# Kernel optimization log

Hardware: AMD Instinct MI355X
Metric: run time of the kernel (lower is better)

The kernel has to match this reference:

```python
import jax, jax.numpy as jnp
import numpy as np

N = 5000        # nodes
F = 7699        # node feature dim (fixed by code)
E = 40000       # edges
ED = 3          # edge_dim (fixed by code)
H1, C1 = 4, 1024
H2, C2 = 1, 1024
NUM_OUT = 128
NEG_SLOPE = 0.2


def _glorot(key, shape):
    fan_in = shape[0]
    return jax.random.normal(key, shape, jnp.float32) / np.float32(np.sqrt(fan_in))


def setup_inputs() -> dict:
    key = jax.random.key(0)
    ks = jax.random.split(key, 16)
    x = jax.random.normal(ks[0], (N, F), jnp.float32)
    src = jax.random.randint(ks[1], (E,), 0, N)
    dst = jax.random.randint(ks[2], (E,), 0, N)
    src = jnp.where(src == dst, (src + 1) % N, src)  # no pre-existing self loops
    edge_index = jnp.stack([src, dst]).astype(jnp.int32)
    edge_attr = jax.random.normal(ks[3], (E, ED), jnp.float32)
    inp = {
        "x": x, "edge_index": edge_index, "edge_attr": edge_attr,
        # GATv2Conv #1: 7699 -> 1024, heads=4, edge_dim=3
        "W1l": _glorot(ks[4], (F, H1 * C1)), "b1l": jnp.zeros((H1 * C1,), jnp.float32),
        "W1r": _glorot(ks[5], (F, H1 * C1)), "b1r": jnp.zeros((H1 * C1,), jnp.float32),
        "W1e": _glorot(ks[6], (ED, H1 * C1)),
        "att1": _glorot(ks[7], (H1, C1)),
        "bias1": jnp.zeros((H1 * C1,), jnp.float32),
        # GATv2Conv #2: 4096 -> 1024, heads=1, edge_dim=3
        "W2l": _glorot(ks[8], (H1 * C1, H2 * C2)), "b2l": jnp.zeros((H2 * C2,), jnp.float32),
        "W2r": _glorot(ks[9], (H1 * C1, H2 * C2)), "b2r": jnp.zeros((H2 * C2,), jnp.float32),
        "W2e": _glorot(ks[10], (ED, H2 * C2)),
        "att2": _glorot(ks[11], (H2, C2)),
        "bias2": jnp.zeros((H2 * C2,), jnp.float32),
        # final Linear(1024, num_outputs)
        "Wlin": _glorot(ks[12], (C2, NUM_OUT)), "blin": jnp.zeros((NUM_OUT,), jnp.float32),
    }
    return inp


def gatv2_layer(x, src, dst, edge_attr, Wl, bl, Wr, br, We, att, bias, heads, out_ch):
    """PyG GATv2Conv with add_self_loops=True, fill_value='mean', concat=True."""
    n = x.shape[0]
    # self-loop edge_attr = mean of incoming edge attrs per node (fill_value='mean')
    deg = jax.ops.segment_sum(jnp.ones((src.shape[0],), jnp.float32), dst, num_segments=n)
    loop_attr = jax.ops.segment_sum(edge_attr, dst, num_segments=n) / jnp.maximum(deg, 1.0)[:, None]
    idx = jnp.arange(n, dtype=src.dtype)
    srcf = jnp.concatenate([src, idx])
    dstf = jnp.concatenate([dst, idx])
    ea = jnp.concatenate([edge_attr, loop_attr], axis=0)
    xl = (x @ Wl + bl).reshape(n, heads, out_ch)   # lin_l (source)
    xr = (x @ Wr + br).reshape(n, heads, out_ch)   # lin_r (target)
    ee = (ea @ We).reshape(-1, heads, out_ch)       # lin_edge (no bias)
    e = jax.nn.leaky_relu(xl[srcf] + xr[dstf] + ee, NEG_SLOPE)  # [E', H, C]
    logit = jnp.einsum('ehc,hc->eh', e, att)                     # [E', H]
    # segment softmax over destination nodes (every node has a self loop)
    m = jax.lax.stop_gradient(jax.ops.segment_max(logit, dstf, num_segments=n))
    a = jnp.exp(logit - m[dstf])
    denom = jax.ops.segment_sum(a, dstf, num_segments=n)
    alpha = a / (denom[dstf] + 1e-16)
    out = jax.ops.segment_sum(alpha[:, :, None] * xl[srcf], dstf, num_segments=n)  # [N,H,C]
    return out.reshape(n, heads * out_ch) + bias


def reference(x, edge_index, edge_attr,
              W1l, b1l, W1r, b1r, W1e, att1, bias1,
              W2l, b2l, W2r, b2r, W2e, att2, bias2,
              Wlin, blin):
    src, dst = edge_index[0], edge_index[1]
    h = gatv2_layer(x, src, dst, edge_attr, W1l, b1l, W1r, b1r, W1e, att1, bias1, H1, C1)
    h = gatv2_layer(h, src, dst, edge_attr, W2l, b2l, W2r, b2r, W2e, att2, bias2, H2, C2)
    return h @ Wlin + blin
```

## Files before the change

kernel.cpp:

```cpp
#include <hip/hip_runtime.h>
#include <cstdint>
#include <cstddef>

#define N_NODES 5000
#define F_IN    7699
#define KP1     7712
#define KT1     241
#define MP      5120
#define E_EDGES 40000
#define EFULL   45000
#define HC1     4096
#define N1      8192
#define HC2     1024
#define N2      2048
#define NOUT    128
#define GM256   (MP / 256)
#define GM128   (MP / 128)

typedef __bf16 bf16x8 __attribute__((ext_vector_type(8)));
typedef float  f32x4  __attribute__((ext_vector_type(4)));
typedef float  f32x16 __attribute__((ext_vector_type(16)));
typedef unsigned short u16x8 __attribute__((ext_vector_type(8)));
typedef _Float16 f16;
typedef _Float16 f16x8 __attribute__((ext_vector_type(8)));

using as1_uchar = unsigned char __attribute__((address_space(1)));
using as3_uchar = unsigned char __attribute__((address_space(3)));

__device__ __forceinline__ unsigned short f2bf(float f) {
  union { float f; unsigned int u; } v; v.f = f;
  return (unsigned short)((v.u + 0x7fffu + ((v.u >> 16) & 1u)) >> 16);
}
__device__ __forceinline__ float bf2f(unsigned short h) {
  union { unsigned int u; float f; } v; v.u = ((unsigned int)h) << 16;
  return v.f;
}

__device__ __forceinline__ void gload16(const void* g, void* l) {
  __builtin_amdgcn_global_load_lds(
      reinterpret_cast<const as1_uchar*>(reinterpret_cast<uintptr_t>(g)),
      reinterpret_cast<as3_uchar*>(reinterpret_cast<uintptr_t>(l)),
      16, 0, 0);
}



__global__ void k_split_x(const float* __restrict__ x, unsigned short* __restrict__ hi,
                          unsigned short* __restrict__ lo) {
  const int C8 = KP1 / 8;
  int ci = blockIdx.x * 256 + threadIdx.x;
  if (ci >= MP * C8) return;
  int r = ci / C8, c8 = ci % C8;
  int c = c8 * 8;
  u16x8 hb, lb;
  #pragma unroll
  for (int j = 0; j < 8; ++j) {
    float v = 0.f;
    if (r < N_NODES && (c + j) < F_IN) v = x[(size_t)r * F_IN + c + j];
    unsigned short h = f2bf(v);
    hb[j] = h; lb[j] = f2bf(v - bf2f(h));
  }
  size_t off = ((size_t)((r >> 7) * KT1 + (c >> 5)) * 4 + ((c >> 3) & 3)) * 1024 + (r & 127) * 8;
  *(u16x8*)&hi[off] = hb;
  *(u16x8*)&lo[off] = lb;
}


__global__ void k_split_w(const float* __restrict__ W,
                          unsigned short* __restrict__ hi, unsigned short* __restrict__ lo,
                          int K, int Nsrc, int c0, int KT, int rowOffset) {
  __shared__ float tile[32][33];
  const int tid = threadIdx.x;
  const int kt = blockIdx.x;
  const int n0 = blockIdx.y * 32;
  #pragma unroll
  for (int i = tid >> 5; i < 32; i += 8) {
    int k = kt * 32 + i;
    tile[i][tid & 31] = (k < K) ? W[(size_t)k * Nsrc + c0 + n0 + (tid & 31)] : 0.f;
  }
  __syncthreads();
  if (tid < 128) {
    const int nn = tid >> 2, kc = (tid & 3) << 3;
    const int n = rowOffset + n0 + nn;
    u16x8 hb, lb;
    #pragma unroll
    for (int j = 0; j < 8; ++j) {
      float v = tile[kc + j][nn];
      unsigned short h = f2bf(v);
      hb[j] = h; lb[j] = f2bf(v - bf2f(h));
    }
    size_t off = ((size_t)((n >> 7) * KT + kt) * 4 + (kc >> 3)) * 1024 + (n & 127) * 8;
    *(u16x8*)&hi[off] = hb;
    *(u16x8*)&lo[off] = lb;
  }
}


template <int OF16>
__global__ __launch_bounds__(512, 2) void k_gemm_big(
    const unsigned short* __restrict__ Ahi, const unsigned short* __restrict__ Alo,
    const unsigned short* __restrict__ Bhi, const unsigned short* __restrict__ Blo,
    void* __restrict__ Cp, const float* __restrict__ bias0, const float* __restrict__ bias1,
    int halfN, int M, int Nc, int ldC, int KT32, int nbn)
{
  __shared__ __align__(16) unsigned short S[4 * 12288];

  const int tid = threadIdx.x;
  const int lane = tid & 63;
  const int w = tid >> 6;
  const int wm = w >> 1, wn = w & 1;

  const int nwg = gridDim.x;
  const int qq = nwg >> 3, rr = nwg & 7;
  const int xcd = blockIdx.x & 7, idx = blockIdx.x >> 3;
  const int wg = (xcd < rr ? xcd * (qq + 1) : rr * (qq + 1) + (xcd - rr) * qq) + idx;
  const int bm = wg / nbn, bn = wg % nbn;

  f32x16 acc[2][2] = {};

  const unsigned short* gsrc[3];
  int dd[3];
  #pragma unroll
  for (int s = 0; s < 3; ++s) {
    const int q = w * 3 + s;
    const unsigned short* base; int dOff; size_t rowoff; int p, hf;
    if (q < 8)       { int r_ = q;      base = Ahi; int t = r_ >> 2; p = (r_ >> 1) & 1; hf = r_ & 1;
                       dOff = t * 2048 + p * 1024 + hf * 512; rowoff = (size_t)(bm * 2 + t) * KT32 * 4096; }
    else if (q < 16) { int r_ = q - 8;  base = Alo; int t = r_ >> 2; p = (r_ >> 1) & 1; hf = r_ & 1;
                       dOff = 4096 + t * 2048 + p * 1024 + hf * 512; rowoff = (size_t)(bm * 2 + t) * KT32 * 4096; }
    else if (q < 20) { int r_ = q - 16; base = Bhi; p = (r_ >> 1) & 1; hf = r_ & 1;
                       dOff = 8192 + p * 1024 + hf * 512; rowoff = (size_t)bn * KT32 * 4096; }
    else             { int r_ = q - 20; base = Blo; p = (r_ >> 1) & 1; hf = r_ & 1;
                       dOff = 10240 + p * 1024 + hf * 512; rowoff = (size_t)bn * KT32 * 4096; }
    gsrc[s] = base + rowoff + p * 1024 + hf * 512 + lane * 8;
    dd[s] = dOff;
  }

  auto stage = [&](int kt16, int bufo) {
    const size_t o = (size_t)kt16 * 2048;
    #pragma unroll
    for (int s = 0; s < 3; ++s) gload16(gsrc[s] + o, &S[bufo + dd[s]]);
  };

  const int r5 = lane & 31, h5 = lane >> 5;
  const int tA = wm >> 1;
  const int rrA = (wm & 1) * 64;
  int ra[2], cb[2];
  #pragma unroll
  for (int i = 0; i < 2; ++i) ra[i] = tA * 2048 + h5 * 1024 + (rrA + i * 32 + r5) * 8;
  #pragma unroll
  for (int j = 0; j < 2; ++j) cb[j] = 8192 + h5 * 1024 + (wn * 64 + j * 32 + r5) * 8;

  struct Frags { bf16x8 ah[2], al[2], bh[2], bl[2]; };
  auto rdfr = [&](Frags& f, int bufo) {
    #pragma unroll
    for (int i = 0; i < 2; ++i) {
      f.ah[i] = *(const bf16x8*)&S[bufo + ra[i]];
      f.al[i] = *(const bf16x8*)&S[bufo + 4096 + ra[i]];
    }
    #pragma unroll
    for (int j = 0; j < 2; ++j) {
      f.bh[j] = *(const bf16x8*)&S[bufo + cb[j]];
      f.bl[j] = *(const bf16x8*)&S[bufo + 2048 + cb[j]];
    }
  };
  auto domfma = [&](Frags& f) {
    __builtin_amdgcn_s_setprio(1);
    #pragma unroll
    for (int j = 0; j < 2; ++j)
      #pragma unroll
      for (int i = 0; i < 2; ++i) {
        acc[i][j] = __builtin_amdgcn_mfma_f32_32x32x16_bf16(f.ah[i], f.bh[j], acc[i][j], 0, 0, 0);
        acc[i][j] = __builtin_amdgcn_mfma_f32_32x32x16_bf16(f.al[i], f.bh[j], acc[i][j], 0, 0, 0);
        acc[i][j] = __builtin_amdgcn_mfma_f32_32x32x16_bf16(f.ah[i], f.bl[j], acc[i][j], 0, 0, 0);
      }
    __builtin_amdgcn_s_setprio(0);
  };

  const int KT16 = KT32 * 2;

  stage(0, 0);
  stage(1, 12288);
  stage(2, 24576);
  asm volatile("s_waitcnt vmcnt(3)" ::: "memory");
  __builtin_amdgcn_s_barrier();
  Frags fA, fB;
  rdfr(fA, 0);

  int o0 = 0, o1 = 12288, o2 = 24576, o3 = 36864;
  for (int kt = 0; kt < KT16; kt += 2) {
    stage((kt + 3 < KT16) ? kt + 3 : KT16 - 1, o3);
    rdfr(fB, o1);
    domfma(fA);
    asm volatile("s_waitcnt vmcnt(3)" ::: "memory");
    __builtin_amdgcn_s_barrier();
    stage((kt + 4 < KT16) ? kt + 4 : KT16 - 1, o0);
    rdfr(fA, o2);
    domfma(fB);
    asm volatile("s_waitcnt vmcnt(3)" ::: "memory");
    __builtin_amdgcn_s_barrier();
    int t0 = o0, t1 = o1;
    o0 = o2; o1 = o3; o2 = t0; o3 = t1;
  }

  #pragma unroll
  for (int i = 0; i < 2; ++i) {
    #pragma unroll
    for (int j = 0; j < 2; ++j) {
      const int gc = bn * 128 + wn * 64 + j * 32 + r5;
      if (gc < Nc) {
        const float bv = (gc < halfN) ? bias0[gc] : bias1[gc - halfN];
        #pragma unroll
        for (int reg = 0; reg < 16; ++reg) {
          const int gr = bm * 256 + wm * 64 + i * 32 + (reg & 3) + 8 * (reg >> 2) + 4 * h5;
          if (gr < M) {
            float v = acc[i][j][reg] + bv;
            if (OF16) ((f16*)Cp)[(size_t)gr * ldC + gc] = (f16)v;
            else      ((float*)Cp)[(size_t)gr * ldC + gc] = v;
          }
        }
      }
    }
  }
}


template <int OF16>
__global__ __launch_bounds__(256, 2) void k_gemm_bb(
    const unsigned short* __restrict__ Ahi, const unsigned short* __restrict__ Alo,
    const unsigned short* __restrict__ Bhi, const unsigned short* __restrict__ Blo,
    void* __restrict__ Cp, const float* __restrict__ bias0, const float* __restrict__ bias1,
    int halfN, int M, int Nc, int ldC, int KT32, int nbn)
{
  __shared__ __align__(16) unsigned short S[4 * 8192];

  const int tid = threadIdx.x;
  const int lane = tid & 63;
  const int w = tid >> 6;
  const int wm = w >> 1, wn = w & 1;

  const int nwg = gridDim.x;
  const int qq = nwg >> 3, rr = nwg & 7;
  const int xcd = blockIdx.x & 7, idx = blockIdx.x >> 3;
  const int wg = (xcd < rr ? xcd * (qq + 1) : rr * (qq + 1) + (xcd - rr) * qq) + idx;
  const int bm = wg / nbn, bn = wg % nbn;

  f32x16 acc[2][2] = {};

  const unsigned short* gbase = (w == 0) ? Ahi : (w == 1) ? Alo : (w == 2) ? Bhi : Blo;
  const int brow = (w < 2) ? bm : bn;
  const unsigned short* gsrc[4];
  int dd[4];
  #pragma unroll
  for (int s = 0; s < 4; ++s) {
    const int p = s >> 1, hf = s & 1;
    gsrc[s] = gbase + (size_t)brow * KT32 * 4096 + p * 1024 + hf * 512 + lane * 8;
    dd[s] = w * 2048 + p * 1024 + hf * 512;
  }

  auto stage = [&](int kt16, int bufo) {
    const size_t o = (size_t)kt16 * 2048;
    #pragma unroll
    for (int s = 0; s < 4; ++s) gload16(gsrc[s] + o, &S[bufo + dd[s]]);
  };

  const int r5 = lane & 31, h5 = lane >> 5;
  int ra[2], cb[2];
  #pragma unroll
  for (int i = 0; i < 2; ++i) ra[i] = h5 * 1024 + (wm * 64 + i * 32 + r5) * 8;
  #pragma unroll
  for (int j = 0; j < 2; ++j) cb[j] = 4096 + h5 * 1024 + (wn * 64 + j * 32 + r5) * 8;

  struct Frags { bf16x8 ah[2], al[2], bh[2], bl[2]; };
  auto rdfr = [&](Frags& f, int bufo) {
    #pragma unroll
    for (int i = 0; i < 2; ++i) {
      f.ah[i] = *(const bf16x8*)&S[bufo + ra[i]];
      f.al[i] = *(const bf16x8*)&S[bufo + 2048 + ra[i]];
    }
    #pragma unroll
    for (int j = 0; j < 2; ++j) {
      f.bh[j] = *(const bf16x8*)&S[bufo + cb[j]];
      f.bl[j] = *(const bf16x8*)&S[bufo + 2048 + cb[j]];
    }
  };
  auto domfma = [&](Frags& f) {
    __builtin_amdgcn_s_setprio(1);
    #pragma unroll
    for (int j = 0; j < 2; ++j)
      #pragma unroll
      for (int i = 0; i < 2; ++i) {
        acc[i][j] = __builtin_amdgcn_mfma_f32_32x32x16_bf16(f.ah[i], f.bh[j], acc[i][j], 0, 0, 0);
        acc[i][j] = __builtin_amdgcn_mfma_f32_32x32x16_bf16(f.al[i], f.bh[j], acc[i][j], 0, 0, 0);
        acc[i][j] = __builtin_amdgcn_mfma_f32_32x32x16_bf16(f.ah[i], f.bl[j], acc[i][j], 0, 0, 0);
      }
    __builtin_amdgcn_s_setprio(0);
  };

  const int KT16 = KT32 * 2;

  stage(0, 0);
  stage(1, 8192);
  stage(2, 16384);
  asm volatile("s_waitcnt vmcnt(4)" ::: "memory");
  __builtin_amdgcn_s_barrier();
  Frags fA, fB;
  rdfr(fA, 0);

  int o0 = 0, o1 = 8192, o2 = 16384, o3 = 24576;
  for (int kt = 0; kt < KT16; kt += 2) {
    stage((kt + 3 < KT16) ? kt + 3 : KT16 - 1, o3);
    rdfr(fB, o1);
    domfma(fA);
    asm volatile("s_waitcnt vmcnt(4)" ::: "memory");
    __builtin_amdgcn_s_barrier();
    stage((kt + 4 < KT16) ? kt + 4 : KT16 - 1, o0);
    rdfr(fA, o2);
    domfma(fB);
    asm volatile("s_waitcnt vmcnt(4)" ::: "memory");
    __builtin_amdgcn_s_barrier();
    int t0 = o0, t1 = o1;
    o0 = o2; o1 = o3; o2 = t0; o3 = t1;
  }

  #pragma unroll
  for (int i = 0; i < 2; ++i) {
    #pragma unroll
    for (int j = 0; j < 2; ++j) {
      const int gc = bn * 128 + wn * 64 + j * 32 + r5;
      if (gc < Nc) {
        const float bv = (gc < halfN) ? bias0[gc] : bias1[gc - halfN];
        #pragma unroll
        for (int reg = 0; reg < 16; ++reg) {
          const int gr = bm * 128 + wm * 64 + i * 32 + (reg & 3) + 8 * (reg >> 2) + 4 * h5;
          if (gr < M) {
            float v = acc[i][j][reg] + bv;
            if (OF16) ((f16*)Cp)[(size_t)gr * ldC + gc] = (f16)v;
            else      ((float*)Cp)[(size_t)gr * ldC + gc] = v;
          }
        }
      }
    }
  }
}


__global__ void k_deg(const int* __restrict__ dst, const float* __restrict__ ea,
                      float* __restrict__ deg, float* __restrict__ lattr, int E) {
  int e = blockIdx.x * 256 + threadIdx.x;
  if (e >= E) return;
  int d = dst[e];
  atomicAdd(&deg[d], 1.f);
  atomicAdd(&lattr[d * 3 + 0], ea[e * 3 + 0]);
  atomicAdd(&lattr[d * 3 + 1], ea[e * 3 + 1]);
  atomicAdd(&lattr[d * 3 + 2], ea[e * 3 + 2]);
}

__global__ void k_lattr_fin(float* __restrict__ lattr, const float* __restrict__ deg, int n) {
  int i = blockIdx.x * 256 + threadIdx.x;
  if (i >= n) return;
  float dv = fmaxf(deg[i], 1.f);
  lattr[i * 3 + 0] /= dv; lattr[i * 3 + 1] /= dv; lattr[i * 3 + 2] /= dv;
}

__global__ void k_eafull(const float* __restrict__ ea, const float* __restrict__ lattr,
                         float* __restrict__ eaf, int E, int n) {
  int e = blockIdx.x * 256 + threadIdx.x;
  if (e >= E + n) return;
  const float* s = (e < E) ? &ea[(size_t)e * 3] : &lattr[(size_t)(e - E) * 3];
  eaf[e * 3 + 0] = s[0]; eaf[e * 3 + 1] = s[1]; eaf[e * 3 + 2] = s[2];
}

__global__ void k_count(const int* __restrict__ dst, int* __restrict__ cnt, int E, int n) {
  int e = blockIdx.x * 256 + threadIdx.x;
  if (e >= E + n) return;
  int d = (e < E) ? dst[e] : (e - E);
  atomicAdd(&cnt[d], 1);
}

__global__ void k_scan(const int* __restrict__ cnt, int* __restrict__ rowptr, int n) {
  int lane = threadIdx.x;
  int run = 0;
  for (int base = 0; base < n; base += 64) {
    int i = base + lane;
    int v = (i < n) ? cnt[i] : 0;
    #pragma unroll
    for (int off = 1; off < 64; off <<= 1) {
      int t = __shfl_up(v, off, 64);
      if (lane >= off) v += t;
    }
    if (i < n) rowptr[i + 1] = run + v;
    run += __shfl(v, 63, 64);
  }
  if (lane == 0) rowptr[0] = 0;
}

__global__ void k_fill(const int* __restrict__ dst, const int* __restrict__ rowptr,
                       int* __restrict__ fillc, int* __restrict__ elist, int E, int n) {
  int e = blockIdx.x * 256 + threadIdx.x;
  if (e >= E + n) return;
  int d = (e < E) ? dst[e] : (e - E);
  int pos = rowptr[d] + atomicAdd(&fillc[d], 1);
  elist[pos] = e;
}


template <int H, int ITERS>
__global__ __launch_bounds__(256) void k_logit_stats(
    const f16* __restrict__ xl, const f16* __restrict__ xr, int strideX,
    const float* __restrict__ eaf, const float* __restrict__ We, const float* __restrict__ att,
    const int* __restrict__ rowptr, const int* __restrict__ elist, const int* __restrict__ src,
    int E, float* __restrict__ logit, float* __restrict__ mb, float* __restrict__ db)
{
  const int n = blockIdx.x;
  const int tid = threadIdx.x;
  constexpr int HC = ITERS * 256;
  float xrv[ITERS], w0[ITERS], w1[ITERS], w2[ITERS], av[ITERS];
  const f16* rr = xr + (size_t)n * strideX;
  #pragma unroll
  for (int i = 0; i < ITERS; ++i) {
    const int hc = tid + (i << 8);
    xrv[i] = (float)rr[hc];
    w0[i] = We[hc]; w1[i] = We[HC + hc]; w2[i] = We[2 * HC + hc];
    av[i] = att[hc];
  }
  const int start = rowptr[n], end = rowptr[n + 1];
  __shared__ float red[H][4];
  const int lane = tid & 63, wv = tid >> 6;
  float mh = -1e30f, sh = 0.f;

  for (int p = start; p < end; ++p) {
    const int e = elist[p];
    const int s = (e < E) ? src[e] : (e - E);
    const float ea0 = eaf[e * 3 + 0], ea1 = eaf[e * 3 + 1], ea2 = eaf[e * 3 + 2];
    const f16* rl = xl + (size_t)s * strideX;
    float acc[H];
    #pragma unroll
    for (int h = 0; h < H; ++h) acc[h] = 0.f;
    #pragma unroll
    for (int i = 0; i < ITERS; ++i) {
      const int hc = tid + (i << 8);
      float v = (float)rl[hc] + xrv[i] + ea0 * w0[i] + ea1 * w1[i] + ea2 * w2[i];
      v = (v > 0.f) ? v : 0.2f * v;
      acc[i >> 2] += v * av[i];
    }
    #pragma unroll
    for (int h = 0; h < H; ++h) {
      float v = acc[h];
      #pragma unroll
      for (int off = 32; off > 0; off >>= 1) v += __shfl_down(v, off, 64);
      if (lane == 0) red[h][wv] = v;
    }
    __syncthreads();
    if (tid < H) {
      const float l = red[tid][0] + red[tid][1] + red[tid][2] + red[tid][3];
      logit[(size_t)e * H + tid] = l;
      const float mn = fmaxf(mh, l);
      sh = sh * __expf(mh - mn) + __expf(l - mn);
      mh = mn;
    }
    __syncthreads();
  }
  if (tid < H) { mb[n * H + tid] = mh; db[n * H + tid] = sh; }
}

template <int H, int NC8, int KTo>
__global__ __launch_bounds__(256) void k_agg(
    const f16* __restrict__ xl, int strideX,
    const int* __restrict__ rowptr, const int* __restrict__ elist, const int* __restrict__ src,
    const float* __restrict__ logit, const float* __restrict__ mb, const float* __restrict__ db,
    const float* __restrict__ bias,
    unsigned short* __restrict__ ohi, unsigned short* __restrict__ olo, int E)
{
  const int n = blockIdx.x;
  const int tid = threadIdx.x;
  constexpr int HC = H * 1024;
  float acc[NC8][8];
  #pragma unroll
  for (int q = 0; q < NC8; ++q)
    #pragma unroll
    for (int j = 0; j < 8; ++j) acc[q][j] = 0.f;
  const int start = rowptr[n], end = rowptr[n + 1];
  float mloc[H], dloc[H];
  #pragma unroll
  for (int h = 0; h < H; ++h) { mloc[h] = mb[n * H + h]; dloc[h] = db[n * H + h] + 1e-16f; }
  for (int p = start; p < end; ++p) {
    const int e = elist[p];
    const int s = (e < E) ? src[e] : (e - E);
    float al[H];
    #pragma unroll
    for (int h = 0; h < H; ++h)
      al[h] = __expf(logit[(size_t)e * H + h] - mloc[h]) / dloc[h];
    const f16* row = xl + (size_t)s * strideX;
    #pragma unroll
    for (int q = 0; q < NC8; ++q) {
      const int c8 = tid + q * 256;
      if (c8 * 8 < HC) {
        float a = (H == 4) ? ((tid & 128) ? al[2 * q + 1] : al[2 * q]) : al[0];
        f16x8 v = *(const f16x8*)(row + c8 * 8);
        #pragma unroll
        for (int j = 0; j < 8; ++j) acc[q][j] += a * (float)v[j];
      }
    }
  }
  #pragma unroll
  for (int q = 0; q < NC8; ++q) {
    const int c8 = tid + q * 256;
    if (c8 * 8 < HC) {
      u16x8 hb, lb;
      #pragma unroll
      for (int j = 0; j < 8; ++j) {
        float v = acc[q][j] + bias[c8 * 8 + j];
        unsigned short h = f2bf(v);
        hb[j] = h; lb[j] = f2bf(v - bf2f(h));
      }
      size_t off = ((size_t)((n >> 7) * KTo + (c8 >> 2)) * 4 + (c8 & 3)) * 1024 + (n & 127) * 8;
      *(u16x8*)&ohi[off] = hb;
      *(u16x8*)&olo[off] = lb;
    }
  }
}


extern "C" void kernel_launch(void* const* d_in, const int* in_sizes, int n_in,
                              void* d_out, int out_size, void* d_ws, size_t ws_size,
                              hipStream_t stream) {
  const float* x    = (const float*)d_in[0];
  const int*   eidx = (const int*)d_in[1];
  const float* eattr= (const float*)d_in[2];
  const float* W1l  = (const float*)d_in[3];
  const float* b1l  = (const float*)d_in[4];
  const float* W1r  = (const float*)d_in[5];
  const float* b1r  = (const float*)d_in[6];
  const float* W1e  = (const float*)d_in[7];
  const float* att1 = (const float*)d_in[8];
  const float* bias1= (const float*)d_in[9];
  const float* W2l  = (const float*)d_in[10];
  const float* b2l  = (const float*)d_in[11];
  const float* W2r  = (const float*)d_in[12];
  const float* b2r  = (const float*)d_in[13];
  const float* W2e  = (const float*)d_in[14];
  const float* att2 = (const float*)d_in[15];
  const float* bias2= (const float*)d_in[16];
  const float* Wlin = (const float*)d_in[17];
  const float* blin = (const float*)d_in[18];
  float* out = (float*)d_out;

  char* ws = (char*)d_ws;
  const int* srcp = eidx;
  const int* dstp = eidx + E_EDGES;

  auto alignup = [](size_t v) { return (v + 255) & ~(size_t)255; };

  size_t mo = 0;
  auto take = [&](size_t sz) { size_t r = mo; mo = alignup(mo + sz); return r; };
  const size_t oLATTR = take((size_t)N_NODES * 3 * 4);
  const size_t oDEG   = take((size_t)N_NODES * 4);
  const size_t oEAF   = take((size_t)EFULL * 3 * 4);
  const size_t oCNT   = take((size_t)N_NODES * 4);
  const size_t oROW   = take((size_t)(N_NODES + 1) * 4);
  const size_t oFILL  = take((size_t)N_NODES * 4);
  const size_t oELIST = take((size_t)EFULL * 4);
  const size_t oLOGIT = take((size_t)EFULL * 4 * 4);
  const size_t oMB    = take((size_t)N_NODES * 4 * 4);
  const size_t oDB    = take((size_t)N_NODES * 4 * 4);
  const size_t oXHI   = take((size_t)MP * KP1 * 2);
  const size_t oXLO   = take((size_t)MP * KP1 * 2);
  const size_t oXLR   = take((size_t)N_NODES * N1 * 2);
  const size_t oBH    = take((size_t)N1 * KP1 * 2);
  const size_t oBL    = take((size_t)N1 * KP1 * 2);
  if (ws_size < mo) return;

  const size_t oH1HI = oXHI;
  const size_t oH1LO = oXLO;
  const size_t oXLR2 = oXLR;
  const size_t oH2HI = oXLR + 32ull * 1024 * 1024;
  const size_t oH2LO = oXLR + 48ull * 1024 * 1024;
  const size_t oB2H  = oBH;
  const size_t oB2L  = oBH + 32ull * 1024 * 1024;
  const size_t oB3H  = oBH;
  const size_t oB3L  = oBH + 1ull * 1024 * 1024;

  unsigned short* XHI  = (unsigned short*)(ws + oXHI);
  unsigned short* XLO  = (unsigned short*)(ws + oXLO);
  f16*            XLR  = (f16*)(ws + oXLR);
  unsigned short* BH   = (unsigned short*)(ws + oBH);
  unsigned short* BL   = (unsigned short*)(ws + oBL);
  float*          LATTR= (float*)(ws + oLATTR);
  float*          DEG  = (float*)(ws + oDEG);
  float*          EAF  = (float*)(ws + oEAF);
  int*            CNT  = (int*)(ws + oCNT);
  int*            ROWP = (int*)(ws + oROW);
  int*            FILLC= (int*)(ws + oFILL);
  int*            ELIST= (int*)(ws + oELIST);
  float*          LOGIT= (float*)(ws + oLOGIT);
  float*          MB   = (float*)(ws + oMB);
  float*          DB   = (float*)(ws + oDB);
  unsigned short* H1HI = (unsigned short*)(ws + oH1HI);
  unsigned short* H1LO = (unsigned short*)(ws + oH1LO);
  f16*            XLR2 = (f16*)(ws + oXLR2);
  unsigned short* H2HI = (unsigned short*)(ws + oH2HI);
  unsigned short* H2LO = (unsigned short*)(ws + oH2LO);
  unsigned short* B2H  = (unsigned short*)(ws + oB2H);
  unsigned short* B2L  = (unsigned short*)(ws + oB2L);
  unsigned short* B3H  = (unsigned short*)(ws + oB3H);
  unsigned short* B3L  = (unsigned short*)(ws + oB3L);

  hipMemsetAsync(ws + oDEG,   0, (size_t)N_NODES * 4, stream);
  hipMemsetAsync(ws + oLATTR, 0, (size_t)N_NODES * 3 * 4, stream);
  hipMemsetAsync(ws + oCNT,   0, (size_t)N_NODES * 4, stream);
  hipMemsetAsync(ws + oFILL,  0, (size_t)N_NODES * 4, stream);

  const int gE  = (E_EDGES + 255) / 256;
  const int gEF = (EFULL + 255) / 256;
  const int gN  = (N_NODES + 255) / 256;

  k_deg<<<gE, 256, 0, stream>>>(dstp, eattr, DEG, LATTR, E_EDGES);
  k_lattr_fin<<<gN, 256, 0, stream>>>(LATTR, DEG, N_NODES);
  k_eafull<<<gEF, 256, 0, stream>>>(eattr, LATTR, EAF, E_EDGES, N_NODES);
  k_count<<<gEF, 256, 0, stream>>>(dstp, CNT, E_EDGES, N_NODES);
  k_scan<<<1, 64, 0, stream>>>(CNT, ROWP, N_NODES);
  k_fill<<<gEF, 256, 0, stream>>>(dstp, ROWP, FILLC, ELIST, E_EDGES, N_NODES);

  k_split_x<<<MP * (KP1 / 8) / 256, 256, 0, stream>>>(x, XHI, XLO);
  k_split_w<<<dim3(KT1, HC1 / 32), 256, 0, stream>>>(W1l, BH, BL, F_IN, HC1, 0, KT1, 0);
  k_split_w<<<dim3(KT1, HC1 / 32), 256, 0, stream>>>(W1r, BH, BL, F_IN, HC1, 0, KT1, HC1);
  k_gemm_big<1><<<GM256 * (N1 / 128), 512, 0, stream>>>(
      XHI, XLO, BH, BL, XLR, b1l, b1r, HC1, N_NODES, N1, N1, KT1, N1 / 128);

  k_logit_stats<4, 16><<<N_NODES, 256, 0, stream>>>(
      XLR, XLR + HC1, N1, EAF, W1e, att1, ROWP, ELIST, srcp, E_EDGES, LOGIT, MB, DB);
  hipMemsetAsync(ws + oH1HI, 0, (size_t)MP * HC1 * 2, stream);
  hipMemsetAsync(ws + oH1LO, 0, (size_t)MP * HC1 * 2, stream);
  k_agg<4, 2, HC1 / 32><<<N_NODES, 256, 0, stream>>>(
      XLR, N1, ROWP, ELIST, srcp, LOGIT, MB, DB, bias1, H1HI, H1LO, E_EDGES);

  k_split_w<<<dim3(HC1 / 32, HC2 / 32), 256, 0, stream>>>(W2l, B2H, B2L, HC1, HC2, 0, HC1 / 32, 0);
  k_split_w<<<dim3(HC1 / 32, HC2 / 32), 256, 0, stream>>>(W2r, B2H, B2L, HC1, HC2, 0, HC1 / 32, HC2);
  k_gemm_bb<1><<<GM128 * (N2 / 128), 256, 0, stream>>>(
      H1HI, H1LO, B2H, B2L, XLR2, b2l, b2r, HC2, N_NODES, N2, N2, HC1 / 32, N2 / 128);

  k_logit_stats<1, 4><<<N_NODES, 256, 0, stream>>>(
      XLR2, XLR2 + HC2, N2, EAF, W2e, att2, ROWP, ELIST, srcp, E_EDGES, LOGIT, MB, DB);
  hipMemsetAsync(ws + oH2HI, 0, (size_t)MP * HC2 * 2, stream);
  hipMemsetAsync(ws + oH2LO, 0, (size_t)MP * HC2 * 2, stream);
  k_agg<1, 1, HC2 / 32><<<N_NODES, 256, 0, stream>>>(
      XLR2, N2, ROWP, ELIST, srcp, LOGIT, MB, DB, bias2, H2HI, H2LO, E_EDGES);

  k_split_w<<<dim3(HC2 / 32, NOUT / 32), 256, 0, stream>>>(Wlin, B3H, B3L, HC2, NOUT, 0, HC2 / 32, 0);
  k_gemm_bb<0><<<GM128 * 1, 256, 0, stream>>>(
      H2HI, H2LO, B3H, B3L, out, blin, blin, NOUT, N_NODES, NOUT, NOUT, HC2 / 32, 1);
}
```

Measured before the change: 2.660 ms.

## Fuse logit/softmax-stats and aggregation into one online-softmax attention kernel

Merges the per-node logit/statistics kernel and the aggregation kernel into a single kernel that uses an online softmax. Each gathered source row is rescaled and accumulated in the same pass that computes its logit. This removes the second gather of xl rows, the logit/max/denominator round trips through global memory, and one launch per layer. In exchange the output is staged through shared memory to keep the packed bf16 hi/lo layout, and there is an extra block barrier plus a per-element rescale on every edge.

```diff
diff --git a/kernel.cpp b/kernel.cpp
--- a/kernel.cpp
+++ b/kernel.cpp
@@ -406,15 +406,20 @@
 
 
 template <int H, int ITERS>
-__global__ __launch_bounds__(256) void k_logit_stats(
+__global__ __launch_bounds__(256) void k_attn(
     const f16* __restrict__ xl, const f16* __restrict__ xr, int strideX,
     const float* __restrict__ eaf, const float* __restrict__ We, const float* __restrict__ att,
     const int* __restrict__ rowptr, const int* __restrict__ elist, const int* __restrict__ src,
-    int E, float* __restrict__ logit, float* __restrict__ mb, float* __restrict__ db)
+    int E, const float* __restrict__ bias,
+    unsigned short* __restrict__ ohi, unsigned short* __restrict__ olo, int KTo)
 {
+  constexpr int HC = ITERS * 256;
   const int n = blockIdx.x;
   const int tid = threadIdx.x;
-  constexpr int HC = ITERS * 256;
+  __shared__ float red[H][4];
+  __shared__ float wbr[H], rbr[H], dsh[H];
+  __shared__ float sx[HC];
+
   float xrv[ITERS], w0[ITERS], w1[ITERS], w2[ITERS], av[ITERS];
   const f16* rr = xr + (size_t)n * strideX;
   #pragma unroll
@@ -424,29 +429,33 @@
     w0[i] = We[hc]; w1[i] = We[HC + hc]; w2[i] = We[2 * HC + hc];
     av[i] = att[hc];
   }
+  float acc[ITERS];
+  #pragma unroll
+  for (int i = 0; i < ITERS; ++i) acc[i] = 0.f;
+  float mh = -1e30f, sh = 0.f;
+  const int lane = tid & 63, wv = tid >> 6;
   const int start = rowptr[n], end = rowptr[n + 1];
-  __shared__ float red[H][4];
-  const int lane = tid & 63, wv = tid >> 6;
-  float mh = -1e30f, sh = 0.f;
 
   for (int p = start; p < end; ++p) {
     const int e = elist[p];
     const int s = (e < E) ? src[e] : (e - E);
     const float ea0 = eaf[e * 3 + 0], ea1 = eaf[e * 3 + 1], ea2 = eaf[e * 3 + 2];
     const f16* rl = xl + (size_t)s * strideX;
-    float acc[H];
-    #pragma unroll
-    for (int h = 0; h < H; ++h) acc[h] = 0.f;
+    float xlv[ITERS];
+    float accL[H];
+    #pragma unroll
+    for (int h = 0; h < H; ++h) accL[h] = 0.f;
     #pragma unroll
     for (int i = 0; i < ITERS; ++i) {
       const int hc = tid + (i << 8);
-      float v = (float)rl[hc] + xrv[i] + ea0 * w0[i] + ea1 * w1[i] + ea2 * w2[i];
+      xlv[i] = (float)rl[hc];
+      float v = xlv[i] + xrv[i] + ea0 * w0[i] + ea1 * w1[i] + ea2 * w2[i];
       v = (v > 0.f) ? v : 0.2f * v;
-      acc[i >> 2] += v * av[i];
+      accL[i >> 2] += v * av[i];
     }
     #pragma unroll
     for (int h = 0; h < H; ++h) {
-      float v = acc[h];
+      float v = accL[h];
       #pragma unroll
       for (int off = 32; off > 0; off >>= 1) v += __shfl_down(v, off, 64);
       if (lane == 0) red[h][wv] = v;
@@ -454,55 +463,31 @@
     __syncthreads();
     if (tid < H) {
       const float l = red[tid][0] + red[tid][1] + red[tid][2] + red[tid][3];
-      logit[(size_t)e * H + tid] = l;
       const float mn = fmaxf(mh, l);
-      sh = sh * __expf(mh - mn) + __expf(l - mn);
+      const float r_ = __expf(mh - mn), w_ = __expf(l - mn);
+      sh = sh * r_ + w_;
       mh = mn;
+      wbr[tid] = w_; rbr[tid] = r_;
     }
     __syncthreads();
-  }
-  if (tid < H) { mb[n * H + tid] = mh; db[n * H + tid] = sh; }
-}
-
-template <int H, int NC8, int KTo>
-__global__ __launch_bounds__(256) void k_agg(
-    const f16* __restrict__ xl, int strideX,
-    const int* __restrict__ rowptr, const int* __restrict__ elist, const int* __restrict__ src,
-    const float* __restrict__ logit, const float* __restrict__ mb, const float* __restrict__ db,
-    const float* __restrict__ bias,
-    unsigned short* __restrict__ ohi, unsigned short* __restrict__ olo, int E)
-{
-  const int n = blockIdx.x;
-  const int tid = threadIdx.x;
-  constexpr int HC = H * 1024;
-  float acc[NC8][8];
-  #pragma unroll
-  for (int q = 0; q < NC8; ++q)
-    #pragma unroll
-    for (int j = 0; j < 8; ++j) acc[q][j] = 0.f;
-  const int start = rowptr[n], end = rowptr[n + 1];
-  float mloc[H], dloc[H];
-  #pragma unroll
-  for (int h = 0; h < H; ++h) { mloc[h] = mb[n * H + h]; dloc[h] = db[n * H + h] + 1e-16f; }
-  for (int p = start; p < end; ++p) {
-    const int e = elist[p];
-    const int s = (e < E) ? src[e] : (e - E);
-    float al[H];
-    #pragma unroll
-    for (int h = 0; h < H; ++h)
-      al[h] = __expf(logit[(size_t)e * H + h] - mloc[h]) / dloc[h];
-    const f16* row = xl + (size_t)s * strideX;
-    #pragma unroll
-    for (int q = 0; q < NC8; ++q) {
-      const int c8 = tid + q * 256;
-      if (c8 * 8 < HC) {
-        float a = (H == 4) ? ((tid & 128) ? al[2 * q + 1] : al[2 * q]) : al[0];
-        f16x8 v = *(const f16x8*)(row + c8 * 8);
-        #pragma unroll
-        for (int j = 0; j < 8; ++j) acc[q][j] += a * (float)v[j];
-      }
-    }
-  }
+    #pragma unroll
+    for (int i = 0; i < ITERS; ++i) {
+      const int h = (H == 4) ? (i >> 2) : 0;
+      acc[i] = acc[i] * rbr[h] + wbr[h] * xlv[i];
+    }
+  }
+
+  if (tid < H) dsh[tid] = sh + 1e-16f;
+  __syncthreads();
+  #pragma unroll
+  for (int i = 0; i < ITERS; ++i) {
+    const int hc = tid + (i << 8);
+    const int h = (H == 4) ? (i >> 2) : 0;
+    sx[hc] = acc[i] / dsh[h] + bias[hc];
+  }
+  __syncthreads();
+
+  constexpr int NC8 = (HC / 8 + 255) / 256;
   #pragma unroll
   for (int q = 0; q < NC8; ++q) {
     const int c8 = tid + q * 256;
@@ -510,7 +495,7 @@
       u16x8 hb, lb;
       #pragma unroll
       for (int j = 0; j < 8; ++j) {
-        float v = acc[q][j] + bias[c8 * 8 + j];
+        float v = sx[c8 * 8 + j];
         unsigned short h = f2bf(v);
         hb[j] = h; lb[j] = f2bf(v - bf2f(h));
       }
@@ -593,9 +578,6 @@
   int*            ROWP = (int*)(ws + oROW);
   int*            FILLC= (int*)(ws + oFILL);
   int*            ELIST= (int*)(ws + oELIST);
-  float*          LOGIT= (float*)(ws + oLOGIT);
-  float*          MB   = (float*)(ws + oMB);
-  float*          DB   = (float*)(ws + oDB);
   unsigned short* H1HI = (unsigned short*)(ws + oH1HI);
   unsigned short* H1LO = (unsigned short*)(ws + oH1LO);
   f16*            XLR2 = (f16*)(ws + oXLR2);
@@ -605,6 +587,7 @@
   unsigned short* B2L  = (unsigned short*)(ws + oB2L);
   unsigned short* B3H  = (unsigned short*)(ws + oB3H);
   unsigned short* B3L  = (unsigned short*)(ws + oB3L);
+  (void)oLOGIT; (void)oMB; (void)oDB;
 
   hipMemsetAsync(ws + oDEG,   0, (size_t)N_NODES * 4, stream);
   hipMemsetAsync(ws + oLATTR, 0, (size_t)N_NODES * 3 * 4, stream);
@@ -628,24 +611,22 @@
   k_gemm_big<1><<<GM256 * (N1 / 128), 512, 0, stream>>>(
       XHI, XLO, BH, BL, XLR, b1l, b1r, HC1, N_NODES, N1, N1, KT1, N1 / 128);
 
-  k_logit_stats<4, 16><<<N_NODES, 256, 0, stream>>>(
-      XLR, XLR + HC1, N1, EAF, W1e, att1, ROWP, ELIST, srcp, E_EDGES, LOGIT, MB, DB);
   hipMemsetAsync(ws + oH1HI, 0, (size_t)MP * HC1 * 2, stream);
   hipMemsetAsync(ws + oH1LO, 0, (size_t)MP * HC1 * 2, stream);
-  k_agg<4, 2, HC1 / 32><<<N_NODES, 256, 0, stream>>>(
-      XLR, N1, ROWP, ELIST, srcp, LOGIT, MB, DB, bias1, H1HI, H1LO, E_EDGES);
+  k_attn<4, 16><<<N_NODES, 256, 0, stream>>>(
+      XLR, XLR + HC1, N1, EAF, W1e, att1, ROWP, ELIST, srcp, E_EDGES,
+      bias1, H1HI, H1LO, HC1 / 32);
 
   k_split_w<<<dim3(HC1 / 32, HC2 / 32), 256, 0, stream>>>(W2l, B2H, B2L, HC1, HC2, 0, HC1 / 32, 0);
   k_split_w<<<dim3(HC1 / 32, HC2 / 32), 256, 0, stream>>>(W2r, B2H, B2L, HC1, HC2, 0, HC1 / 32, HC2);
   k_gemm_bb<1><<<GM128 * (N2 / 128), 256, 0, stream>>>(
       H1HI, H1LO, B2H, B2L, XLR2, b2l, b2r, HC2, N_NODES, N2, N2, HC1 / 32, N2 / 128);
 
-  k_logit_stats<1, 4><<<N_NODES, 256, 0, stream>>>(
-      XLR2, XLR2 + HC2, N2, EAF, W2e, att2, ROWP, ELIST, srcp, E_EDGES, LOGIT, MB, DB);
   hipMemsetAsync(ws + oH2HI, 0, (size_t)MP * HC2 * 2, stream);
   hipMemsetAsync(ws + oH2LO, 0, (size_t)MP * HC2 * 2, stream);
-  k_agg<1, 1, HC2 / 32><<<N_NODES, 256, 0, stream>>>(
-      XLR2, N2, ROWP, ELIST, srcp, LOGIT, MB, DB, bias2, H2HI, H2LO, E_EDGES);
+  k_attn<1, 4><<<N_NODES, 256, 0, stream>>>(
+      XLR2, XLR2 + HC2, N2, EAF, W2e, att2, ROWP, ELIST, srcp, E_EDGES,
+      bias2, H2HI, H2LO, HC2 / 32);
 
   k_split_w<<<dim3(HC2 / 32, NOUT / 32), 256, 0, stream>>>(Wlin, B3H, B3L, HC2, NOUT, 0, HC2 / 32, 0);
   k_gemm_bb<0><<<GM128 * 1, 256, 0, stream>>>(
```

After: 2.588 ms. 2.7% less time.
